# Kernel tuning notes

Measured on AMD Instinct MI355X. Metric: run time of the kernel, lower is better.

## Reference

```python
import jax, jax.numpy as jnp
import numpy as np

SUB_NO = 64
SYN_BASIS_NO = 3
T_HIST = 200
T_DATA = 100000


def setup_inputs() -> dict:
    key = jax.random.key(0)
    ks = jax.random.split(key, 5)
    # strictly-lower-triangular adjacency: each subunit integrates from ancestors
    C_den = jnp.tril((jax.random.uniform(ks[0], (SUB_NO, SUB_NO)) < 0.15).astype(jnp.float32), k=-1)
    S_conv = jax.random.normal(ks[1], (T_DATA, SUB_NO), dtype=jnp.float32)
    Y_ancest = 0.1 * jax.random.normal(ks[2], (T_DATA, SUB_NO), dtype=jnp.float32)
    # sparse binary spike trains
    Z_ancest = (jax.random.uniform(ks[3], (T_DATA, SUB_NO)) < 0.05).astype(jnp.float32)
    V_o = jnp.full((1,), -69.0, dtype=jnp.float32)
    W_sub = jnp.full((SUB_NO,), 0.25, dtype=jnp.float32)
    theta_syn = jnp.zeros((SUB_NO,), dtype=jnp.float32)
    K_spike = jnp.full((SUB_NO, SYN_BASIS_NO), 0.01, dtype=jnp.float32)
    tau_spike = jnp.arange(1.6, 1.6 + SYN_BASIS_NO, dtype=jnp.float32)
    delta_spike = jnp.zeros((SUB_NO,), dtype=jnp.float32)
    return {"S_conv": S_conv, "Y_ancest": Y_ancest, "Z_ancest": Z_ancest,
            "C_den": C_den, "V_o": V_o, "W_sub": W_sub, "theta_syn": theta_syn,
            "K_spike": K_spike, "tau_spike": tau_spike, "delta_spike": delta_spike,
            "T_hist": T_HIST}


def _ancest_kernel(K_spike, tau_spike, delta_spike, T_hist):
    # t[s, k] = max(k - delta_s, 0); kern[s, k] = sum_b (t/tau_b) exp(-t/tau_b) K[s,b]
    t = jnp.arange(T_hist, dtype=jnp.float32)[None, :] - delta_spike[:, None]
    t = jnp.maximum(t, 0.0)                                  # [sub, T_hist]
    tau = jnp.exp(tau_spike)                                 # [basis]
    t_tau = t[:, None, :] / tau[None, :, None]               # [sub, basis, T_hist]
    kern = jnp.sum(t_tau * jnp.exp(-t_tau) * K_spike[:, :, None], axis=1)
    return kern                                              # [sub, T_hist]


def reference(S_conv, Y_ancest, Z_ancest, C_den, V_o, W_sub, theta_syn,
              K_spike, tau_spike, delta_spike, T_hist):
    T_data, sub_no = S_conv.shape
    kern = _ancest_kernel(K_spike, tau_spike, delta_spike, T_hist)
    kern_f = jnp.flip(kern, axis=1)                          # matches torch.flip

    # spike_ancest[t, s, k] = sum_j C_den[s,j] Z_pad[t+k, j]  ->  precontract once
    Zc = Z_ancest @ C_den.T                                  # [T, sub]
    Zc_pad = jnp.concatenate([jnp.zeros((T_hist, sub_no), Zc.dtype), Zc], axis=0)
    # depthwise VALID conv over time: filtered[t, s] = sum_k kern_f[s,k] Zc_pad[t+k, s]
    out = jax.lax.conv_general_dilated(
        Zc_pad.T[None],                                      # [1, sub, T+T_hist]
        kern_f[:, None, :],                                  # [sub, 1, T_hist]
        window_strides=(1,), padding='VALID',
        feature_group_count=sub_no,
        dimension_numbers=('NCH', 'OIH', 'NCH'))
    filtered = out[0, :, :T_data].T                          # [T, sub]

    raw = Y_ancest @ C_den.T                                 # [T, sub]
    X_in = S_conv + theta_syn + filtered + raw
    final_Y = jax.nn.sigmoid(X_in) * W_sub + V_o
    return final_Y
```

## Files before the change

kernel.cpp:

```cpp
#include <hip/hip_runtime.h>

#define SUBS  64
#define GUARD 256
#define LB    32
#define JT    8
#define LSTR  136

typedef _Float16 f16x8 __attribute__((ext_vector_type(8)));
typedef float    f32x4 __attribute__((ext_vector_type(4)));

__device__ inline f16x8 ld_frag(const float* p) {
    float4 a = *(const float4*)p;
    float4 b = *(const float4*)(p + 4);
    f16x8 f;
    f[0]=(_Float16)a.x; f[1]=(_Float16)a.y; f[2]=(_Float16)a.z; f[3]=(_Float16)a.w;
    f[4]=(_Float16)b.x; f[5]=(_Float16)b.y; f[6]=(_Float16)b.z; f[7]=(_Float16)b.w;
    return f;
}
__device__ inline uint pkh2(float a, float b) {
    union { _Float16 h[2]; uint u; } p;
    p.h[0] = (_Float16)a; p.h[1] = (_Float16)b; return p.u;
}

#define STEP3(u)                                                                 \
    _Pragma("unroll")                                                            \
    for (int b = 0; b < 3; ++b) {                                                \
        const float yn = fmaf(twr[b], y1[b], fmaf(mr2[b], y2[b], cr[b] * (u)));  \
        y2[b] = y1[b]; y1[b] = yn;                                               \
    }
#define PAIRW(wrd) {                                                             \
    union { uint u; _Float16 h[2]; } w_; w_.u = (wrd);                           \
    STEP3((float)w_.h[0]);                                                       \
    STEP3((float)w_.h[1]); }

__global__ __launch_bounds__(256, 4) void k_mm(
    const float* __restrict__ Z, const float* __restrict__ Y,
    const float* __restrict__ S, const float* __restrict__ C,
    const float* __restrict__ theta,
    const float* __restrict__ K_spike, const float* __restrict__ tau_spike,
    const float* __restrict__ delta_spike,
    _Float16* __restrict__ Zt, _Float16* __restrict__ Bt,
    float* __restrict__ fb, int T, int rgz, int NB)
{
    __shared__ _Float16 ztl[SUBS * LSTR];
    __shared__ _Float16 ytl[SUBS * LSTR];
    const int tid  = threadIdx.x;
    const int lane = tid & 63;
    const int wv   = tid >> 6;
    const int lr   = lane & 15;
    const int lg   = lane >> 4;
    const int t0b  = blockIdx.x * 128;

    int dl = (int)rintf(delta_spike[lane]);
    dl = min(max(dl, 0), 30);
    const bool alldl0 = __all(dl == 0);

    if (blockIdx.x == 0) {
        for (int idx = tid; idx < JT * 512; idx += 256) fb[idx] = 0.f;
    }
    if (!alldl0) {
        if (blockIdx.x < 8) {
            const int tile = blockIdx.x * 4 + wv;
            uint4 z4 = {0, 0, 0, 0};
            ((uint4*)Zt)[(size_t)tile * 64 + lane] = z4;
            ((uint4*)Bt)[(size_t)tile * 64 + lane] = z4;
        } else if (blockIdx.x < 18) {
            const int tile = rgz + (blockIdx.x - 8) * 4 + wv;
            uint4 z4 = {0, 0, 0, 0};
            ((uint4*)Zt)[(size_t)tile * 64 + lane] = z4;
            ((uint4*)Bt)[(size_t)tile * 64 + lane] = z4;
        }
    }

    f16x8 bfr[4][2];
    #pragma unroll
    for (int nt = 0; nt < 4; ++nt)
        #pragma unroll
        for (int ks = 0; ks < 2; ++ks)
            bfr[nt][ks] = ld_frag(&C[(lr + 16 * nt) * 64 + ks * 32 + lg * 8]);

    float th4[4];
    #pragma unroll
    for (int nt = 0; nt < 4; ++nt) th4[nt] = theta[lr + 16 * nt];

    #pragma unroll
    for (int g = 0; g < 2; ++g) {
        const int t0 = t0b + wv * 32 + g * 16;
        const int rowA = t0 + lr;
        const bool okA = rowA < T;
        f16x8 az[2], ay[2];
        #pragma unroll
        for (int ks = 0; ks < 2; ++ks) {
            if (okA) {
                az[ks] = ld_frag(&Z[(size_t)rowA * 64 + ks * 32 + lg * 8]);
                ay[ks] = ld_frag(&Y[(size_t)rowA * 64 + ks * 32 + lg * 8]);
            } else {
                az[ks] = (f16x8)(_Float16)0.f;
                ay[ks] = (f16x8)(_Float16)0.f;
            }
        }

        f32x4 accZ[4], accY[4];
        #pragma unroll
        for (int nt = 0; nt < 4; ++nt) { accZ[nt] = (f32x4){0,0,0,0}; accY[nt] = (f32x4){0,0,0,0}; }
        #pragma unroll
        for (int nt = 0; nt < 4; ++nt) {
            #pragma unroll
            for (int ks = 0; ks < 2; ++ks) {
                accZ[nt] = __builtin_amdgcn_mfma_f32_16x16x32_f16(az[ks], bfr[nt][ks], accZ[nt], 0, 0, 0);
                accY[nt] = __builtin_amdgcn_mfma_f32_16x16x32_f16(ay[ks], bfr[nt][ks], accY[nt], 0, 0, 0);
            }
        }

        #pragma unroll
        for (int nt = 0; nt < 4; ++nt) {
            const int sc = lr + 16 * nt;
            #pragma unroll
            for (int r = 0; r < 4; ++r) {
                const int t = t0 + lg * 4 + r;
                if (t < T) accY[nt][r] += S[(size_t)t * 64 + sc] + th4[nt];
            }
        }

        #pragma unroll
        for (int nt = 0; nt < 4; ++nt) {
            const int sc = lr + 16 * nt;
            const int lt = wv * 32 + g * 16 + lg * 4;
            uint2 pz, py;
            pz.x = pkh2(accZ[nt][0], accZ[nt][1]);
            pz.y = pkh2(accZ[nt][2], accZ[nt][3]);
            py.x = pkh2(accY[nt][0], accY[nt][1]);
            py.y = pkh2(accY[nt][2], accY[nt][3]);
            *(uint2*)&ztl[sc * LSTR + lt] = pz;
            *(uint2*)&ytl[sc * LSTR + lt] = py;
        }
    }

    __syncthreads();

    const int gbase = (GUARD >> 3) + blockIdx.x * 16;
    #pragma unroll
    for (int it = 0; it < 4; ++it) {
        const int chunk = it * 256 + tid;
        const int row = chunk & 63;
        const int col = chunk >> 6;
        const int tb  = t0b + col * 8;
        if (tb + 7 < T) {
            ((uint4*)Zt)[(size_t)(gbase + col) * 64 + row] =
                *(const uint4*)&ztl[row * LSTR + col * 8];
            ((uint4*)Bt)[(size_t)(gbase + col) * 64 + row] =
                *(const uint4*)&ytl[row * LSTR + col * 8];
        } else {
            union { ushort u[8]; uint4 v; } vz, vb;
            #pragma unroll
            for (int h = 0; h < 8; ++h) {
                const bool ok = (tb + h < T);
                vz.u[h] = ok ? ((const ushort*)ztl)[row * LSTR + col * 8 + h] : (ushort)0;
                vb.u[h] = ok ? ((const ushort*)ytl)[row * LSTR + col * 8 + h] : (ushort)0;
            }
            ((uint4*)Zt)[(size_t)(gbase + col) * 64 + row] = vz.v;
            ((uint4*)Bt)[(size_t)(gbase + col) * 64 + row] = vb.v;
        }
    }

    const int grun = blockIdx.x * 4 + wv;
    if (grun < NB) {
        float twr[3], mr2[3], cr[3];
        #pragma unroll
        for (int b = 0; b < 3; ++b) {
            const float tau = __expf(tau_spike[b]);
            const float r   = __expf(-1.0f / tau);
            twr[b] = 2.0f * r;
            mr2[b] = -r * r;
            cr[b]  = K_spike[lane * 3 + b] / tau * r;
        }
        const uint* zr = (const uint*)ztl + lane * (LSTR / 2) + wv * 16;
        float y1[3] = {0.f, 0.f, 0.f}, y2[3] = {0.f, 0.f, 0.f};
        #pragma unroll
        for (int k = 0; k < 16; ++k) PAIRW(zr[k]);
        float* fout = fb + (size_t)(grun + JT) * 512 + lane * 8;
        *(float4*)fout       = make_float4(y1[0], y2[0], y1[1], y2[1]);
        *(float2*)(fout + 4) = make_float2(y1[2], y2[2]);
    }
}

#define EMIT(o, f) {                                                             \
    const int t_ = t0 + (o);                                                     \
    if (t_ < T) {                                                                \
        union { uint u; _Float16 h[2]; } wb_; wb_.u = bwd[(o) >> 1];             \
        const float xin_ = (float)wb_.h[(o) & 1] + (f);                          \
        const float sig_ = 1.0f / (1.0f + __expf(-xin_));                        \
        out[(size_t)t_ * 64 + s] = fmaf(sig_, wsub, vo);                         \
    } }

__global__ __launch_bounds__(256, 4) void k_iir2(
    const _Float16* __restrict__ Zt, const _Float16* __restrict__ Bt,
    const float* __restrict__ K_spike, const float* __restrict__ tau_spike,
    const float* __restrict__ delta_spike,
    const float* __restrict__ W, const float* __restrict__ Vo,
    const float* __restrict__ fb, float* __restrict__ out, int T, int NB)
{
    const int tid = threadIdx.x;
    const int s   = tid & 63;
    const int wv  = tid >> 6;
    const int i   = blockIdx.x * 4 + wv;
    if (i >= NB) return;
    const int t0 = i * LB;

    float twr[3], mr2[3], cr[3], taus[3];
    #pragma unroll
    for (int b = 0; b < 3; ++b) {
        const float tau = __expf(tau_spike[b]);
        taus[b] = tau;
        const float r = __expf(-1.0f / tau);
        twr[b] = 2.0f * r;
        mr2[b] = -r * r;
        cr[b]  = K_spike[s * 3 + b] / tau * r;
    }
    int dl = (int)rintf(delta_spike[s]);
    dl = min(max(dl, 0), 30);
    const float wsub = W[s];
    const float vo   = Vo[0];

    if (__all(dl == 0)) {
        float aL[3], bL[3], cL[3], dL[3];
        #pragma unroll
        for (int b = 0; b < 3; ++b) {
            const float r   = 0.5f * twr[b];
            const float rm1 = __expf(-(float)(LB - 1) / taus[b]);
            const float rl  = rm1 * r;
            const float rp  = rl * r;
            aL[b] = (float)(LB + 1) * rl;
            bL[b] = -(float)LB * rp;
            cL[b] = (float)LB * rm1;
            dL[b] = -(float)(LB - 1) * rl;
        }
        float y1[3], y2[3];
        {
            const float* fq = fb + (size_t)i * 512 + s * 8;
            const float4 lo = *(const float4*)fq;
            const float2 hi = *(const float2*)(fq + 4);
            y1[0] = lo.x; y2[0] = lo.y; y1[1] = lo.z; y2[1] = lo.w;
            y1[2] = hi.x; y2[2] = hi.y;
        }
        #pragma unroll
        for (int j = 7; j >= 1; --j) {
            const float* fq = fb + (size_t)(i + JT - j) * 512 + s * 8;
            const float4 lo = *(const float4*)fq;
            const float2 hi = *(const float2*)(fq + 4);
            const float f1[3] = { lo.x, lo.z, hi.x };
            const float f2[3] = { lo.y, lo.w, hi.y };
            #pragma unroll
            for (int b = 0; b < 3; ++b) {
                const float n1 = fmaf(aL[b], y1[b], fmaf(bL[b], y2[b], f1[b]));
                const float n2 = fmaf(cL[b], y1[b], fmaf(dL[b], y2[b], f2[b]));
                y1[b] = n1; y2[b] = n2;
            }
        }

        const uint4* xb = (const uint4*)Zt + (size_t)(32 + 4 * i) * 64 + s;
        const uint4 x0 = xb[0], x1 = xb[64], x2 = xb[128], x3 = xb[192];
        const uint4* bb = (const uint4*)Bt + (size_t)(32 + 4 * i) * 64 + s;
        const uint4 b0 = bb[0], b1 = bb[64], b2 = bb[128], b3 = bb[192];

        const uint xw[15]  = { x0.x, x0.y, x0.z, x0.w, x1.x, x1.y, x1.z, x1.w,
                               x2.x, x2.y, x2.z, x2.w, x3.x, x3.y, x3.z };
        const uint bwd[16] = { b0.x, b0.y, b0.z, b0.w, b1.x, b1.y, b1.z, b1.w,
                               b2.x, b2.y, b2.z, b2.w, b3.x, b3.y, b3.z, b3.w };

        EMIT(0, y2[0] + y2[1] + y2[2]);
        EMIT(1, y1[0] + y1[1] + y1[2]);
        #pragma unroll
        for (int w = 0; w < 15; ++w) {
            union { uint u; _Float16 h[2]; } wx; wx.u = xw[w];
            STEP3((float)wx.h[0]);
            EMIT(2 + 2 * w, y1[0] + y1[1] + y1[2]);
            STEP3((float)wx.h[1]);
            EMIT(3 + 2 * w, y1[0] + y1[1] + y1[2]);
        }
    } else {
        float y1[3] = {0.f, 0.f, 0.f}, y2[3] = {0.f, 0.f, 0.f};
        const int xi0 = t0 - 226 - dl;
        for (int k = 0; k < 224 + LB; ++k) {
            const int h = GUARD + xi0 + k;
            const float u = (float)Zt[(size_t)(h >> 3) * 512 + s * 8 + (h & 7)];
            STEP3(u);
            const int o = k - 224;
            if (o >= 0) {
                const int t = t0 + o;
                if (t < T) {
                    const int hy = GUARD + t;
                    const float bv = (float)Bt[(size_t)(hy >> 3) * 512 + s * 8 + (hy & 7)];
                    const float xin = bv + y1[0] + y1[1] + y1[2];
                    const float sig = 1.0f / (1.0f + __expf(-xin));
                    out[(size_t)t * 64 + s] = fmaf(sig, wsub, vo);
                }
            }
        }
    }
}

extern "C" void kernel_launch(void* const* d_in, const int* in_sizes, int n_in,
                              void* d_out, int out_size, void* d_ws, size_t ws_size,
                              hipStream_t stream)
{
    const float* S     = (const float*)d_in[0];
    const float* Y     = (const float*)d_in[1];
    const float* Z     = (const float*)d_in[2];
    const float* C     = (const float*)d_in[3];
    const float* Vo    = (const float*)d_in[4];
    const float* W     = (const float*)d_in[5];
    const float* theta = (const float*)d_in[6];
    const float* K     = (const float*)d_in[7];
    const float* tau   = (const float*)d_in[8];
    const float* delta = (const float*)d_in[9];
    const int T  = in_sizes[0] / SUBS;
    const int NB = (T + LB - 1) / LB;

    const int rgz    = (GUARD + T + 7) >> 3;
    const int ntiles = rgz + 44;
    _Float16* Zt = (_Float16*)d_ws;
    _Float16* Bt = (_Float16*)((char*)d_ws + (size_t)ntiles * 1024);
    float*    fb = (float*)((char*)d_ws + (size_t)ntiles * 2048);

    k_mm<<<(T + 127) / 128, 256, 0, stream>>>(Z, Y, S, C, theta, K, tau, delta,
                                              Zt, Bt, fb, T, rgz, NB);
    k_iir2<<<(NB + 3) / 4, 256, 0, stream>>>(Zt, Bt, K, tau, delta, W, Vo, fb,
                                             (float*)d_out, T, NB);
}
```

Baseline: 52.66 us.

## Move S_conv+theta addition from matmul kernel into IIR output kernel

The S_conv plus theta add moves out of the first (MFMA) kernel and into the second (IIR/sigmoid) kernel, which now reads S directly and packs it to fp16 pairs per thread. The first kernel also runs its per-wave segment recurrence before the global store of transposed tiles, so that compute overlaps the stores. The goal is to lighten and shorten the first kernel and rebalance memory traffic between the two launches. In exchange the second kernel does strided 4-byte loads of S per lane (stride 256 B), and S is rounded to fp16 before use, which adds precision loss.

```diff
diff --git a/kernel.cpp b/kernel.cpp
--- a/kernel.cpp
+++ b/kernel.cpp
@@ -35,11 +35,10 @@
 
 __global__ __launch_bounds__(256, 4) void k_mm(
     const float* __restrict__ Z, const float* __restrict__ Y,
-    const float* __restrict__ S, const float* __restrict__ C,
-    const float* __restrict__ theta,
+    const float* __restrict__ C,
     const float* __restrict__ K_spike, const float* __restrict__ tau_spike,
     const float* __restrict__ delta_spike,
-    _Float16* __restrict__ Zt, _Float16* __restrict__ Bt,
+    _Float16* __restrict__ Zt, _Float16* __restrict__ Yt,
     float* __restrict__ fb, int T, int rgz, int NB)
 {
     __shared__ _Float16 ztl[SUBS * LSTR];
@@ -63,12 +62,12 @@
             const int tile = blockIdx.x * 4 + wv;
             uint4 z4 = {0, 0, 0, 0};
             ((uint4*)Zt)[(size_t)tile * 64 + lane] = z4;
-            ((uint4*)Bt)[(size_t)tile * 64 + lane] = z4;
+            ((uint4*)Yt)[(size_t)tile * 64 + lane] = z4;
         } else if (blockIdx.x < 18) {
             const int tile = rgz + (blockIdx.x - 8) * 4 + wv;
             uint4 z4 = {0, 0, 0, 0};
             ((uint4*)Zt)[(size_t)tile * 64 + lane] = z4;
-            ((uint4*)Bt)[(size_t)tile * 64 + lane] = z4;
+            ((uint4*)Yt)[(size_t)tile * 64 + lane] = z4;
         }
     }
 
@@ -78,10 +77,6 @@
         #pragma unroll
         for (int ks = 0; ks < 2; ++ks)
             bfr[nt][ks] = ld_frag(&C[(lr + 16 * nt) * 64 + ks * 32 + lg * 8]);
-
-    float th4[4];
-    #pragma unroll
-    for (int nt = 0; nt < 4; ++nt) th4[nt] = theta[lr + 16 * nt];
 
     #pragma unroll
     for (int g = 0; g < 2; ++g) {
@@ -109,16 +104,6 @@
             for (int ks = 0; ks < 2; ++ks) {
                 accZ[nt] = __builtin_amdgcn_mfma_f32_16x16x32_f16(az[ks], bfr[nt][ks], accZ[nt], 0, 0, 0);
                 accY[nt] = __builtin_amdgcn_mfma_f32_16x16x32_f16(ay[ks], bfr[nt][ks], accY[nt], 0, 0, 0);
-            }
-        }
-
-        #pragma unroll
-        for (int nt = 0; nt < 4; ++nt) {
-            const int sc = lr + 16 * nt;
-            #pragma unroll
-            for (int r = 0; r < 4; ++r) {
-                const int t = t0 + lg * 4 + r;
-                if (t < T) accY[nt][r] += S[(size_t)t * 64 + sc] + th4[nt];
             }
         }
 
@@ -138,6 +123,26 @@
 
     __syncthreads();
 
+    const int grun = blockIdx.x * 4 + wv;
+    if (grun < NB) {
+        float twr[3], mr2[3], cr[3];
+        #pragma unroll
+        for (int b = 0; b < 3; ++b) {
+            const float tau = __expf(tau_spike[b]);
+            const float r   = __expf(-1.0f / tau);
+            twr[b] = 2.0f * r;
+            mr2[b] = -r * r;
+            cr[b]  = K_spike[lane * 3 + b] / tau * r;
+        }
+        const uint* zr = (const uint*)ztl + lane * (LSTR / 2) + wv * 16;
+        float y1[3] = {0.f, 0.f, 0.f}, y2[3] = {0.f, 0.f, 0.f};
+        #pragma unroll
+        for (int k = 0; k < 16; ++k) PAIRW(zr[k]);
+        float* fout = fb + (size_t)(grun + JT) * 512 + lane * 8;
+        *(float4*)fout       = make_float4(y1[0], y2[0], y1[1], y2[1]);
+        *(float2*)(fout + 4) = make_float2(y1[2], y2[2]);
+    }
+
     const int gbase = (GUARD >> 3) + blockIdx.x * 16;
     #pragma unroll
     for (int it = 0; it < 4; ++it) {
@@ -148,55 +153,37 @@
         if (tb + 7 < T) {
             ((uint4*)Zt)[(size_t)(gbase + col) * 64 + row] =
                 *(const uint4*)&ztl[row * LSTR + col * 8];
-            ((uint4*)Bt)[(size_t)(gbase + col) * 64 + row] =
+            ((uint4*)Yt)[(size_t)(gbase + col) * 64 + row] =
                 *(const uint4*)&ytl[row * LSTR + col * 8];
         } else {
-            union { ushort u[8]; uint4 v; } vz, vb;
+            union { ushort u[8]; uint4 v; } vz, vy;
             #pragma unroll
             for (int h = 0; h < 8; ++h) {
                 const bool ok = (tb + h < T);
                 vz.u[h] = ok ? ((const ushort*)ztl)[row * LSTR + col * 8 + h] : (ushort)0;
-                vb.u[h] = ok ? ((const ushort*)ytl)[row * LSTR + col * 8 + h] : (ushort)0;
+                vy.u[h] = ok ? ((const ushort*)ytl)[row * LSTR + col * 8 + h] : (ushort)0;
             }
             ((uint4*)Zt)[(size_t)(gbase + col) * 64 + row] = vz.v;
-            ((uint4*)Bt)[(size_t)(gbase + col) * 64 + row] = vb.v;
-        }
-    }
-
-    const int grun = blockIdx.x * 4 + wv;
-    if (grun < NB) {
-        float twr[3], mr2[3], cr[3];
-        #pragma unroll
-        for (int b = 0; b < 3; ++b) {
-            const float tau = __expf(tau_spike[b]);
-            const float r   = __expf(-1.0f / tau);
-            twr[b] = 2.0f * r;
-            mr2[b] = -r * r;
-            cr[b]  = K_spike[lane * 3 + b] / tau * r;
-        }
-        const uint* zr = (const uint*)ztl + lane * (LSTR / 2) + wv * 16;
-        float y1[3] = {0.f, 0.f, 0.f}, y2[3] = {0.f, 0.f, 0.f};
-        #pragma unroll
-        for (int k = 0; k < 16; ++k) PAIRW(zr[k]);
-        float* fout = fb + (size_t)(grun + JT) * 512 + lane * 8;
-        *(float4*)fout       = make_float4(y1[0], y2[0], y1[1], y2[1]);
-        *(float2*)(fout + 4) = make_float2(y1[2], y2[2]);
+            ((uint4*)Yt)[(size_t)(gbase + col) * 64 + row] = vy.v;
+        }
     }
 }
 
 #define EMIT(o, f) {                                                             \
     const int t_ = t0 + (o);                                                     \
     if (t_ < T) {                                                                \
-        union { uint u; _Float16 h[2]; } wb_; wb_.u = bwd[(o) >> 1];             \
-        const float xin_ = (float)wb_.h[(o) & 1] + (f);                          \
+        union { uint u; _Float16 h[2]; } wy_; wy_.u = ywd[(o) >> 1];             \
+        union { uint u; _Float16 h[2]; } wp_; wp_.u = spk[(o) >> 1];             \
+        const float xin_ = (float)wy_.h[(o) & 1] + (float)wp_.h[(o) & 1] + (f);  \
         const float sig_ = 1.0f / (1.0f + __expf(-xin_));                        \
         out[(size_t)t_ * 64 + s] = fmaf(sig_, wsub, vo);                         \
     } }
 
 __global__ __launch_bounds__(256, 4) void k_iir2(
-    const _Float16* __restrict__ Zt, const _Float16* __restrict__ Bt,
+    const _Float16* __restrict__ Zt, const _Float16* __restrict__ Yt,
+    const float* __restrict__ S,
     const float* __restrict__ K_spike, const float* __restrict__ tau_spike,
-    const float* __restrict__ delta_spike,
+    const float* __restrict__ delta_spike, const float* __restrict__ theta,
     const float* __restrict__ W, const float* __restrict__ Vo,
     const float* __restrict__ fb, float* __restrict__ out, int T, int NB)
 {
@@ -219,10 +206,19 @@
     }
     int dl = (int)rintf(delta_spike[s]);
     dl = min(max(dl, 0), 30);
+    const float th   = theta[s];
     const float wsub = W[s];
     const float vo   = Vo[0];
 
     if (__all(dl == 0)) {
+        uint spk[16];
+        #pragma unroll
+        for (int p = 0; p < 16; ++p) {
+            const int t1 = min(t0 + 2 * p,     T - 1);
+            const int t2 = min(t0 + 2 * p + 1, T - 1);
+            spk[p] = pkh2(S[(size_t)t1 * 64 + s] + th, S[(size_t)t2 * 64 + s] + th);
+        }
+
         float aL[3], bL[3], cL[3], dL[3];
         #pragma unroll
         for (int b = 0; b < 3; ++b) {
@@ -260,13 +256,13 @@
 
         const uint4* xb = (const uint4*)Zt + (size_t)(32 + 4 * i) * 64 + s;
         const uint4 x0 = xb[0], x1 = xb[64], x2 = xb[128], x3 = xb[192];
-        const uint4* bb = (const uint4*)Bt + (size_t)(32 + 4 * i) * 64 + s;
-        const uint4 b0 = bb[0], b1 = bb[64], b2 = bb[128], b3 = bb[192];
+        const uint4* yb = (const uint4*)Yt + (size_t)(32 + 4 * i) * 64 + s;
+        const uint4 yv0 = yb[0], yv1 = yb[64], yv2 = yb[128], yv3 = yb[192];
 
         const uint xw[15]  = { x0.x, x0.y, x0.z, x0.w, x1.x, x1.y, x1.z, x1.w,
                                x2.x, x2.y, x2.z, x2.w, x3.x, x3.y, x3.z };
-        const uint bwd[16] = { b0.x, b0.y, b0.z, b0.w, b1.x, b1.y, b1.z, b1.w,
-                               b2.x, b2.y, b2.z, b2.w, b3.x, b3.y, b3.z, b3.w };
+        const uint ywd[16] = { yv0.x, yv0.y, yv0.z, yv0.w, yv1.x, yv1.y, yv1.z, yv1.w,
+                               yv2.x, yv2.y, yv2.z, yv2.w, yv3.x, yv3.y, yv3.z, yv3.w };
 
         EMIT(0, y2[0] + y2[1] + y2[2]);
         EMIT(1, y1[0] + y1[1] + y1[2]);
@@ -290,8 +286,9 @@
                 const int t = t0 + o;
                 if (t < T) {
                     const int hy = GUARD + t;
-                    const float bv = (float)Bt[(size_t)(hy >> 3) * 512 + s * 8 + (hy & 7)];
-                    const float xin = bv + y1[0] + y1[1] + y1[2];
+                    const float yc = (float)Yt[(size_t)(hy >> 3) * 512 + s * 8 + (hy & 7)];
+                    const float xin = yc + S[(size_t)t * 64 + s] + th
+                                      + y1[0] + y1[1] + y1[2];
                     const float sig = 1.0f / (1.0f + __expf(-xin));
                     out[(size_t)t * 64 + s] = fmaf(sig, wsub, vo);
                 }
@@ -320,11 +317,11 @@
     const int rgz    = (GUARD + T + 7) >> 3;
     const int ntiles = rgz + 44;
     _Float16* Zt = (_Float16*)d_ws;
-    _Float16* Bt = (_Float16*)((char*)d_ws + (size_t)ntiles * 1024);
+    _Float16* Yt = (_Float16*)((char*)d_ws + (size_t)ntiles * 1024);
     float*    fb = (float*)((char*)d_ws + (size_t)ntiles * 2048);
 
-    k_mm<<<(T + 127) / 128, 256, 0, stream>>>(Z, Y, S, C, theta, K, tau, delta,
-                                              Zt, Bt, fb, T, rgz, NB);
-    k_iir2<<<(NB + 3) / 4, 256, 0, stream>>>(Zt, Bt, K, tau, delta, W, Vo, fb,
-                                             (float*)d_out, T, NB);
-}
+    k_mm<<<(T + 127) / 128, 256, 0, stream>>>(Z, Y, C, K, tau, delta,
+                                              Zt, Yt, fb, T, rgz, NB);
+    k_iir2<<<(NB + 3) / 4, 256, 0, stream>>>(Zt, Yt, S, K, tau, delta, theta,
+                                             W, Vo, fb, (float*)d_out, T, NB);
+}
```

Result: slower. 55.57 us (+5.5%).
